# Kernel tuning notes

Hardware: AMD Instinct MI355X
Metric: run time of the kernel (lower is better)

Reference implementation:

```python
import jax, jax.numpy as jnp
import numpy as np

N = 50000        # nodes
E = 400000       # edges
F_IN = 128       # node feature dim
NEG_SLOPE = 0.2  # PyG GATConv default


def setup_inputs() -> dict:
    key = jax.random.key(0)
    ks = jax.random.split(key, 24)
    p = lambda k, shape: (jax.random.normal(k, shape, dtype=jnp.float32) * 0.1)
    return {
        "x": jax.random.normal(ks[0], (N, F_IN), dtype=jnp.float32),
        "edge_index": jax.random.randint(ks[1], (2, E), 0, N, dtype=jnp.int32),
        "edge_attr": jax.random.normal(ks[2], (E, 1), dtype=jnp.float32),
        "year": jax.random.normal(ks[3], (E, 1), dtype=jnp.float32),
        "quarter": jax.random.normal(ks[4], (E, 1), dtype=jnp.float32),
        "W1": p(ks[5], (4 * 128, F_IN)), "a1s": p(ks[6], (4, 128)), "a1d": p(ks[7], (4, 128)), "b1": jnp.zeros((512,), jnp.float32),
        "W2": p(ks[8], (4 * 32, 512)), "a2s": p(ks[9], (4, 32)), "a2d": p(ks[10], (4, 32)), "b2": jnp.zeros((128,), jnp.float32),
        "W3": p(ks[11], (1 * 8, 128)), "a3s": p(ks[12], (1, 8)), "a3d": p(ks[13], (1, 8)), "b3": jnp.zeros((8,), jnp.float32),
        # fc1: 8*2 + 1 + 2 = 19 -> 16 ; fc2: 16 -> 1
        "fc1_w": p(ks[14], (16, 19)), "fc1_b": jnp.zeros((16,), jnp.float32),
        "fc2_w": p(ks[15], (1, 16)), "fc2_b": jnp.zeros((1,), jnp.float32),
    }


def gat_conv(x, src, dst, W, a_s, a_d, b):
    """PyG GATConv (concat=True, self-loops already in src/dst, no dropout)."""
    H, C = a_s.shape
    n = x.shape[0]
    h = (x @ W.T).reshape(n, H, C)                      # [N,H,C]
    s = jnp.einsum("nhc,hc->nh", h, a_s)                # alpha_src per node
    d = jnp.einsum("nhc,hc->nh", h, a_d)                # alpha_dst per node
    e = jax.nn.leaky_relu(s[src] + d[dst], NEG_SLOPE)   # [E',H]
    m = jax.ops.segment_max(e, dst, num_segments=n)     # segment softmax over dst
    ex = jnp.exp(e - m[dst])
    den = jax.ops.segment_sum(ex, dst, num_segments=n)
    alpha = ex / den[dst]                               # [E',H]
    out = jax.ops.segment_sum(alpha[:, :, None] * h[src], dst, num_segments=n)
    return out.reshape(n, H * C) + b


def reference(x, edge_index, edge_attr, year, quarter,
              W1, a1s, a1d, b1, W2, a2s, a2d, b2, W3, a3s, a3d, b3,
              fc1_w, fc1_b, fc2_w, fc2_b):
    n = x.shape[0]
    loops = jnp.arange(n, dtype=edge_index.dtype)       # add_self_loops=True
    src = jnp.concatenate([edge_index[0], loops])
    dst = jnp.concatenate([edge_index[1], loops])
    h = jax.nn.elu(gat_conv(x, src, dst, W1, a1s, a1d, b1))
    h = jax.nn.elu(gat_conv(h, src, dst, W2, a2s, a2d, b2))
    h = jax.nn.elu(gat_conv(h, src, dst, W3, a3s, a3d, b3))
    z = jnp.concatenate([h[edge_index[0]], h[edge_index[1]], edge_attr, year, quarter], axis=1)
    z = jax.nn.relu(z @ fc1_w.T + fc1_b)
    return (z @ fc2_w.T + fc2_b).squeeze(-1)            # [E]
```

## Files before the change

kernel.cpp:

```cpp
#include <hip/hip_runtime.h>
#include <hip/hip_bf16.h>

#define NN 50000
#define EE 400000
#define EP 450000

typedef __attribute__((ext_vector_type(8))) short short8;
typedef __attribute__((ext_vector_type(4))) float f32x4;

__device__ __forceinline__ float us2f(unsigned short u) {
    unsigned int x = ((unsigned int)u) << 16;
    union { unsigned int i; float f; } c; c.i = x; return c.f;
}
__device__ __forceinline__ unsigned short f2bfu(float f) {
    union { float f; unsigned int u; } c; c.f = f;
    unsigned int r = c.u + 0x7FFFu + ((c.u >> 16) & 1u);
    return (unsigned short)(r >> 16);
}
__device__ __forceinline__ unsigned int pack2bf(float lo, float hi) {
    return (unsigned int)f2bfu(lo) | ((unsigned int)f2bfu(hi) << 16);
}
__device__ __forceinline__ float lrelu_exp(float x) {
    x = x > 0.f ? x : 0.2f * x;
    return __expf(x);
}


#define DEGB 1758
#define CVTB 512
__global__ void prep_kernel(const int* __restrict__ ei, int* __restrict__ deg,
                            const float* __restrict__ W1, const float* __restrict__ W2,
                            __hip_bfloat16* __restrict__ pw1, __hip_bfloat16* __restrict__ pw2,
                            const float* __restrict__ a1s, const float* __restrict__ a1d,
                            float* __restrict__ usd) {
    int b = blockIdx.x;
    if (b < DEGB) {
        int e = b * 256 + threadIdx.x;
        if (e >= EP) return;
        int dst = (e < EE) ? ei[EE + e] : e - EE;
        atomicAdd(&deg[dst], 1);
    } else if (b < DEGB + CVTB) {
        int i = (b - DEGB) * 256 + threadIdx.x;
        if (i < 65536) {
            int n = i >> 7, k = i & 127;
            int idx = ((n >> 4) * 4 + (k >> 5)) * 512 + ((k & 31) >> 3) * 128 + (n & 15) * 8 + (k & 7);
            pw1[idx] = __float2bfloat16(W1[i]);
        } else {
            int j = i - 65536;
            int n = j >> 9, k = j & 511;
            int idx = ((n >> 4) * 16 + (k >> 5)) * 512 + ((k & 31) >> 3) * 128 + (n & 15) * 8 + (k & 7);
            pw2[idx] = __float2bfloat16(W2[j]);
        }
    } else {
        int t = (b - DEGB - CVTB) * 256 + threadIdx.x;
        if (t >= 1024) return;
        int row = t >> 7, k = t & 127;
        int hh = row & 3;
        const float* av = (row < 4) ? (a1s + hh * 128) : (a1d + hh * 128);
        const float* wp = W1 + (size_t)(hh * 128) * 128 + k;
        float acc = 0.f;
        for (int c = 0; c < 128; c++) acc += av[c] * wp[(size_t)c * 128];
        usd[t] = acc;
    }
}

__global__ void cvtx_sd(const float* __restrict__ x, const float* __restrict__ usd,
                        __hip_bfloat16* __restrict__ xb,
                        float* __restrict__ s, float* __restrict__ d, int M) {
    __shared__ float us_s[1024];
    for (int i = threadIdx.x; i < 1024; i += 256) us_s[i] = usd[i];
    __syncthreads();
    int wave = threadIdx.x >> 6, lane = threadIdx.x & 63;
    int m0 = blockIdx.x * 64 + wave * 16;
    int r = lane & 15, quad = lane >> 4;
    int am = m0 + r; if (am >= M) am = M - 1;
    const float* xp = x + (size_t)am * 128 + quad * 8;
    float xv[32];
#pragma unroll
    for (int kk = 0; kk < 4; kk++) {
        float4 a = *(const float4*)(xp + kk * 32);
        float4 bq = *(const float4*)(xp + kk * 32 + 4);
        xv[kk*8+0]=a.x;  xv[kk*8+1]=a.y;  xv[kk*8+2]=a.z;  xv[kk*8+3]=a.w;
        xv[kk*8+4]=bq.x; xv[kk*8+5]=bq.y; xv[kk*8+6]=bq.z; xv[kk*8+7]=bq.w;
        short8 o;
        o[0]=(short)f2bfu(a.x);  o[1]=(short)f2bfu(a.y);
        o[2]=(short)f2bfu(a.z);  o[3]=(short)f2bfu(a.w);
        o[4]=(short)f2bfu(bq.x); o[5]=(short)f2bfu(bq.y);
        o[6]=(short)f2bfu(bq.z); o[7]=(short)f2bfu(bq.w);
        *(short8*)(xb + (size_t)am * 128 + quad * 8 + kk * 32) = o;
    }
    float acc[8];
#pragma unroll
    for (int o = 0; o < 8; o++) {
        const float* up = us_s + o * 128 + quad * 8;
        float a = 0.f;
#pragma unroll
        for (int kk = 0; kk < 4; kk++)
#pragma unroll
            for (int j = 0; j < 8; j++) a += xv[kk*8+j] * up[kk*32+j];
        acc[o] = a;
    }
#pragma unroll
    for (int o = 0; o < 8; o++) {
        acc[o] += __shfl_xor(acc[o], 16, 64);
        acc[o] += __shfl_xor(acc[o], 32, 64);
    }
    int m = m0 + r;
    if (quad == 0 && m < M) {
#pragma unroll
        for (int hh = 0; hh < 4; hh++) { s[m*4+hh] = acc[hh]; d[m*4+hh] = acc[4+hh]; }
    }
}

#define SCB 49
__global__ void scan1_kernel(const int* __restrict__ deg, int* __restrict__ bsum) {
    __shared__ int red[256];
    int b = blockIdx.x, t = threadIdx.x;
    int base = b * 1024 + t * 4;
    int s = 0;
    if (base + 3 < NN) { int4 v = *(const int4*)(deg + base); s = v.x + v.y + v.z + v.w; }
    else { for (int i = base; i < NN; i++) s += deg[i]; }
    red[t] = s;
    __syncthreads();
    for (int off = 128; off > 0; off >>= 1) {
        if (t < off) red[t] += red[t + off];
        __syncthreads();
    }
    if (t == 0) bsum[b] = red[0];
}

__global__ void scan2_kernel(const int* __restrict__ deg, const int* __restrict__ bsum,
                             int* __restrict__ offsets) {
    __shared__ int lsum[256];
    int b = blockIdx.x, t = threadIdx.x;
    int boff = 0;
    for (int i = 0; i < b; i++) boff += bsum[i];
    int base = b * 1024 + t * 4;
    int4 v = {0, 0, 0, 0};
    if (base + 3 < NN) v = *(const int4*)(deg + base);
    else {
        if (base < NN)     v.x = deg[base];
        if (base + 1 < NN) v.y = deg[base + 1];
        if (base + 2 < NN) v.z = deg[base + 2];
        if (base + 3 < NN) v.w = deg[base + 3];
    }
    int s = v.x + v.y + v.z + v.w;
    lsum[t] = s;
    __syncthreads();
    for (int off = 1; off < 256; off <<= 1) {
        int val = (t >= off) ? lsum[t - off] : 0;
        __syncthreads();
        lsum[t] += val;
        __syncthreads();
    }
    int ex = boff + (t ? lsum[t - 1] : 0);
    if (base < NN)     offsets[base]     = ex;
    if (base + 1 < NN) offsets[base + 1] = ex + v.x;
    if (base + 2 < NN) offsets[base + 2] = ex + v.x + v.y;
    if (base + 3 < NN) offsets[base + 3] = ex + v.x + v.y + v.z;
    if (b == SCB - 1 && t == 255) offsets[NN] = boff + lsum[255];
}

__global__ void fill_kernel(const int* __restrict__ ei, const int* __restrict__ offsets,
                            int* __restrict__ cursor,
                            const float* __restrict__ s1, const float* __restrict__ d1,
                            int* __restrict__ elist, float* __restrict__ welist) {
    int e = blockIdx.x * blockDim.x + threadIdx.x;
    if (e >= EP) return;
    int src, dst;
    if (e < EE) { src = ei[e]; dst = ei[EE + e]; } else { src = dst = e - EE; }
    int pos = atomicAdd(&cursor[dst], 1);
    int j = offsets[dst] + pos;
    elist[j] = src;
    float4 sv = *(const float4*)(s1 + (size_t)src * 4);
    float4 dv = *(const float4*)(d1 + (size_t)dst * 4);
    float4 w;
    w.x = lrelu_exp(sv.x + dv.x);
    w.y = lrelu_exp(sv.y + dv.y);
    w.z = lrelu_exp(sv.z + dv.z);
    w.w = lrelu_exp(sv.w + dv.w);
    *(float4*)(welist + (size_t)j * 4) = w;
}

__device__ __forceinline__ void acc_edge(float (&den)[4], float (&acc)[8],
                                         float4 w, unsigned int x) {
    float x0 = us2f((unsigned short)x), x1 = us2f((unsigned short)(x >> 16));
    den[0] += w.x; den[1] += w.y; den[2] += w.z; den[3] += w.w;
    acc[0] += w.x * x0; acc[1] += w.x * x1;
    acc[2] += w.y * x0; acc[3] += w.y * x1;
    acc[4] += w.z * x0; acc[5] += w.z * x1;
    acc[6] += w.w * x0; acc[7] += w.w * x1;
}

__global__ void l1_fused(
        const int* __restrict__ elist, const int* __restrict__ offsets,
        const float* __restrict__ wl,
        const __hip_bfloat16* __restrict__ xb,
        const __hip_bfloat16* __restrict__ pW1,
        const float* __restrict__ b,
        __hip_bfloat16* __restrict__ pact) {
    __shared__ unsigned short frag[16 * 520];
    int w = threadIdx.x >> 6, lane = threadIdx.x & 63;
    int m0 = blockIdx.x * 16;
    int nA = m0 + 2 * w;

    int ja  = __builtin_amdgcn_readfirstlane(offsets[nA]);
    int jA1 = __builtin_amdgcn_readfirstlane(offsets[nA + 1]);
    int jB1 = __builtin_amdgcn_readfirstlane(offsets[nA + 2]);
    int jb = jA1;

    float dA[4] = {0.f,0.f,0.f,0.f}, dB[4] = {0.f,0.f,0.f,0.f};
    float aA[8] = {0.f,0.f,0.f,0.f,0.f,0.f,0.f,0.f};
    float aB[8] = {0.f,0.f,0.f,0.f,0.f,0.f,0.f,0.f};
    const unsigned short* xp = (const unsigned short*)xb + lane * 2;
    const float4* wl4 = (const float4*)wl;

    while (ja + 2 <= jA1 && jb + 2 <= jB1) {
        int s0 = elist[ja], s1 = elist[ja + 1];
        int s2 = elist[jb], s3 = elist[jb + 1];
        float4 w0 = wl4[ja], w1 = wl4[ja + 1];
        float4 w2 = wl4[jb], w3 = wl4[jb + 1];
        unsigned int x0 = *(const unsigned int*)(xp + (size_t)s0 * 128);
        unsigned int x1 = *(const unsigned int*)(xp + (size_t)s1 * 128);
        unsigned int x2 = *(const unsigned int*)(xp + (size_t)s2 * 128);
        unsigned int x3 = *(const unsigned int*)(xp + (size_t)s3 * 128);
        acc_edge(dA, aA, w0, x0); acc_edge(dA, aA, w1, x1);
        acc_edge(dB, aB, w2, x2); acc_edge(dB, aB, w3, x3);
        ja += 2; jb += 2;
    }
    while (ja + 2 <= jA1) {
        int s0 = elist[ja], s1 = elist[ja + 1];
        float4 w0 = wl4[ja], w1 = wl4[ja + 1];
        unsigned int x0 = *(const unsigned int*)(xp + (size_t)s0 * 128);
        unsigned int x1 = *(const unsigned int*)(xp + (size_t)s1 * 128);
        acc_edge(dA, aA, w0, x0); acc_edge(dA, aA, w1, x1);
        ja += 2;
    }
    while (jb + 2 <= jB1) {
        int s0 = elist[jb], s1 = elist[jb + 1];
        float4 w0 = wl4[jb], w1 = wl4[jb + 1];
        unsigned int x0 = *(const unsigned int*)(xp + (size_t)s0 * 128);
        unsigned int x1 = *(const unsigned int*)(xp + (size_t)s1 * 128);
        acc_edge(dB, aB, w0, x0); acc_edge(dB, aB, w1, x1);
        jb += 2;
    }
    if (ja < jA1) {
        int s0 = elist[ja]; float4 w0 = wl4[ja];
        unsigned int x0 = *(const unsigned int*)(xp + (size_t)s0 * 128);
        acc_edge(dA, aA, w0, x0);
    }
    if (jb < jB1) {
        int s0 = elist[jb]; float4 w0 = wl4[jb];
        unsigned int x0 = *(const unsigned int*)(xp + (size_t)s0 * 128);
        acc_edge(dB, aB, w0, x0);
    }

    {
        int c0 = lane * 2;
        int fq = c0 >> 5;
        int sub = (c0 & 31) >> 3;
        unsigned int* f32p = (unsigned int*)frag;
        int base0 = fq * 260 + sub * 64 + (c0 & 7) / 2;
        {
            int rowp = (2 * w) ^ (sub << 2);
            int base = base0 + rowp * 4;
            float i0 = 1.f/dA[0], i1 = 1.f/dA[1], i2 = 1.f/dA[2], i3 = 1.f/dA[3];
            f32p[base]            = pack2bf(aA[0]*i0, aA[1]*i0);
            f32p[base + 4 * 260]  = pack2bf(aA[2]*i1, aA[3]*i1);
            f32p[base + 8 * 260]  = pack2bf(aA[4]*i2, aA[5]*i2);
            f32p[base + 12 * 260] = pack2bf(aA[6]*i3, aA[7]*i3);
        }
        {
            int rowp = (2 * w + 1) ^ (sub << 2);
            int base = base0 + rowp * 4;
            float i0 = 1.f/dB[0], i1 = 1.f/dB[1], i2 = 1.f/dB[2], i3 = 1.f/dB[3];
            f32p[base]            = pack2bf(aB[0]*i0, aB[1]*i0);
            f32p[base + 4 * 260]  = pack2bf(aB[2]*i1, aB[3]*i1);
            f32p[base + 8 * 260]  = pack2bf(aB[4]*i2, aB[5]*i2);
            f32p[base + 12 * 260] = pack2bf(aB[6]*i3, aB[7]*i3);
        }
    }
    __syncthreads();

    int hh = w >> 1, half = w & 1;
    int r = lane & 15, quad = lane >> 4;
    int lsub = lane >> 4, lrow = lane & 15;
    int prow = lrow ^ (lsub << 2);
    const unsigned short* fb = frag + lsub * 128 + prow * 8;
    short8 afrag[4];
#pragma unroll
    for (int kk = 0; kk < 4; kk++)
        afrag[kk] = *(const short8*)(fb + (hh * 4 + kk) * 520);
#pragma unroll
    for (int t = 0; t < 4; t++) {
        int nb = half * 64 + t * 16;
        const __hip_bfloat16* bp = pW1 + ((size_t)(hh * 8 + (nb >> 4)) * 4) * 512 + lane * 8;
        f32x4 acc = {0.f, 0.f, 0.f, 0.f};
#pragma unroll
        for (int kk = 0; kk < 4; kk++) {
            short8 bfr = *(const short8*)(bp + kk * 512);
            acc = __builtin_amdgcn_mfma_f32_16x16x32_bf16(afrag[kk], bfr, acc, 0, 0, 0);
        }
        int n0 = hh * 128 + nb;
        float bias = b[n0 + r];
        int kk2 = (n0 + r) >> 5;
        int sub2 = ((nb & 16) + r) >> 3;
        __hip_bfloat16* op = pact + ((size_t)blockIdx.x * 16 + kk2) * 512
                           + sub2 * 128 + (r & 7);
#pragma unroll
        for (int i = 0; i < 4; i++) {
            float v = acc[i] + bias;
            v = v > 0.f ? v : (__expf(v) - 1.0f);
            op[(quad * 4 + i) * 8] = __float2bfloat16(v);
        }
    }
}

__global__ void gemm_l2(const __hip_bfloat16* __restrict__ pA,
                        const __hip_bfloat16* __restrict__ pW2,
                        const float* __restrict__ as_, const float* __restrict__ ad_,
                        __hip_bfloat16* __restrict__ Cb,
                        float* __restrict__ s, float* __restrict__ d, int M) {
    int hh = threadIdx.x >> 6, lane = threadIdx.x & 63;
    int m0 = blockIdx.x * 16;
    int r = lane & 15, quad = lane >> 4;
    const __hip_bfloat16* ap  = pA + (size_t)(m0 >> 4) * 16 * 512 + lane * 8;
    const __hip_bfloat16* bp0 = pW2 + (size_t)(hh * 2) * 16 * 512 + lane * 8;
    const __hip_bfloat16* bp1 = bp0 + 16 * 512;
    f32x4 acc0 = {0.f, 0.f, 0.f, 0.f}, acc1 = {0.f, 0.f, 0.f, 0.f};
#pragma unroll
    for (int kk = 0; kk < 16; kk++) {
        short8 af = *(const short8*)(ap + kk * 512);
        short8 b0 = *(const short8*)(bp0 + kk * 512);
        short8 b1 = *(const short8*)(bp1 + kk * 512);
        acc0 = __builtin_amdgcn_mfma_f32_16x16x32_bf16(af, b0, acc0, 0, 0, 0);
        acc1 = __builtin_amdgcn_mfma_f32_16x16x32_bf16(af, b1, acc1, 0, 0, 0);
    }
    int n0 = hh * 32;
    float as0 = as_[n0 + r],      ad0 = ad_[n0 + r];
    float as1 = as_[n0 + 16 + r], ad1 = ad_[n0 + 16 + r];
    float sacc[4], dacc[4];
#pragma unroll
    for (int i = 0; i < 4; i++) {
        int m = m0 + quad * 4 + i;
        Cb[(size_t)m * 128 + n0 + r]      = __float2bfloat16(acc0[i]);
        Cb[(size_t)m * 128 + n0 + 16 + r] = __float2bfloat16(acc1[i]);
        sacc[i] = acc0[i] * as0 + acc1[i] * as1;
        dacc[i] = acc0[i] * ad0 + acc1[i] * ad1;
    }
#pragma unroll
    for (int mask = 1; mask <= 8; mask <<= 1) {
#pragma unroll
        for (int i = 0; i < 4; i++) {
            sacc[i] += __shfl_xor(sacc[i], mask, 64);
            dacc[i] += __shfl_xor(dacc[i], mask, 64);
        }
    }
    if (r == 0) {
#pragma unroll
        for (int i = 0; i < 4; i++) {
            int m = m0 + quad * 4 + i;
            s[m * 4 + hh] = sacc[i]; d[m * 4 + hh] = dacc[i];
        }
    }
}

__global__ void gather_l2_g8(const int* __restrict__ elist, const int* __restrict__ offsets,
                             const float* __restrict__ s2, const float* __restrict__ d2,
                             const __hip_bfloat16* __restrict__ h,
                             const float* __restrict__ b,
                             const float* __restrict__ W3,
                             const float* __restrict__ a3s, const float* __restrict__ a3d,
                             __hip_bfloat16* __restrict__ h3,
                             float* __restrict__ s3, float* __restrict__ d3) {
    int gid = blockIdx.x * blockDim.x + threadIdx.x;
    if (gid >= NN * 64) return;
    int node = gid >> 6;
    int lane = gid & 63;
    int c0 = lane * 2;
    int hh = lane >> 4;
    int j0 = __builtin_amdgcn_readfirstlane(offsets[node]);
    int j1 = __builtin_amdgcn_readfirstlane(offsets[node + 1]);
    float dv = d2[node * 4 + hh];
    float den = 0.f, acc0 = 0.f, acc1 = 0.f;
    const unsigned short* hp = (const unsigned short*)h + c0;
    int j = j0;
    for (; j + 4 <= j1; j += 4) {
        int sA = elist[j], sB = elist[j+1], sC = elist[j+2], sD = elist[j+3];
        float eA = s2[sA * 4 + hh] + dv, eB = s2[sB * 4 + hh] + dv;
        float eC = s2[sC * 4 + hh] + dv, eD = s2[sD * 4 + hh] + dv;
        unsigned int vA = *(const unsigned int*)(hp + (size_t)sA * 128);
        unsigned int vB = *(const unsigned int*)(hp + (size_t)sB * 128);
        unsigned int vC = *(const unsigned int*)(hp + (size_t)sC * 128);
        unsigned int vD = *(const unsigned int*)(hp + (size_t)sD * 128);
        float wA = lrelu_exp(eA), wB = lrelu_exp(eB);
        float wC = lrelu_exp(eC), wD = lrelu_exp(eD);
        den += (wA + wB) + (wC + wD);
        acc0 += wA * us2f((unsigned short)vA) + wB * us2f((unsigned short)vB)
              + wC * us2f((unsigned short)vC) + wD * us2f((unsigned short)vD);
        acc1 += wA * us2f((unsigned short)(vA >> 16)) + wB * us2f((unsigned short)(vB >> 16))
              + wC * us2f((unsigned short)(vC >> 16)) + wD * us2f((unsigned short)(vD >> 16));
    }
    for (; j < j1; j++) {
        int sE = elist[j];
        float ww = lrelu_exp(s2[sE * 4 + hh] + dv);
        unsigned int v = *(const unsigned int*)(hp + (size_t)sE * 128);
        den += ww;
        acc0 += ww * us2f((unsigned short)v);
        acc1 += ww * us2f((unsigned short)(v >> 16));
    }
    float inv = 1.0f / den;
    float v0 = acc0 * inv + b[c0];
    float v1 = acc1 * inv + b[c0 + 1];
    v0 = v0 > 0.f ? v0 : (__expf(v0) - 1.0f);
    v1 = v1 > 0.f ? v1 : (__expf(v1) - 1.0f);
    float part[8];
#pragma unroll
    for (int c = 0; c < 8; c++) {
        float2 wv = *(const float2*)(W3 + c * 128 + c0);
        part[c] = v0 * wv.x + v1 * wv.y;
    }
#pragma unroll
    for (int mask = 1; mask < 64; mask <<= 1) {
#pragma unroll
        for (int c = 0; c < 8; c++) part[c] += __shfl_xor(part[c], mask, 64);
    }
    if (lane < 8) h3[(size_t)node * 8 + lane] = __float2bfloat16(part[lane]);
    if (lane == 0) {
        float sv = 0.f, dvv = 0.f;
#pragma unroll
        for (int c = 0; c < 8; c++) { sv += part[c] * a3s[c]; dvv += part[c] * a3d[c]; }
        s3[node] = sv; d3[node] = dvv;
    }
}

__global__ void gather_l3(const int* __restrict__ elist, const int* __restrict__ offsets,
                          const float* __restrict__ s3, const float* __restrict__ d3,
                          const __hip_bfloat16* __restrict__ h,
                          const float* __restrict__ b,
                          __hip_bfloat16* __restrict__ act) {
    int gid = blockIdx.x * blockDim.x + threadIdx.x;
    if (gid >= NN * 8) return;
    int node = gid >> 3, t = gid & 7;
    int j0 = offsets[node], j1 = offsets[node + 1];
    float dnode = d3[node];
    float den = 0.f, acc = 0.f;
    const unsigned short* hp = (const unsigned short*)h + t;
    int j = j0;
    for (; j + 4 <= j1; j += 4) {
        int sA = elist[j], sB = elist[j+1], sC = elist[j+2], sD = elist[j+3];
        float wA = lrelu_exp(s3[sA] + dnode), wB = lrelu_exp(s3[sB] + dnode);
        float wC = lrelu_exp(s3[sC] + dnode), wD = lrelu_exp(s3[sD] + dnode);
        float xA = us2f(hp[(size_t)sA * 8]);
        float xB = us2f(hp[(size_t)sB * 8]);
        float xC = us2f(hp[(size_t)sC * 8]);
        float xD = us2f(hp[(size_t)sD * 8]);
        den += (wA + wB) + (wC + wD);
        acc += wA * xA + wB * xB + wC * xC + wD * xD;
    }
    for (; j < j1; j++) {
        int sE = elist[j];
        float w = lrelu_exp(s3[sE] + dnode);
        den += w;
        acc += w * us2f(hp[(size_t)sE * 8]);
    }
    float v = acc / den + b[t];
    v = v > 0.f ? v : (__expf(v) - 1.0f);
    act[(size_t)node * 8 + t] = __float2bfloat16(v);
}

__global__ void mlp_kernel(const int* __restrict__ ei,
                           const __hip_bfloat16* __restrict__ act3,
                           const float* __restrict__ ea,
                           const float* __restrict__ yr,
                           const float* __restrict__ qt,
                           const float* __restrict__ fc1w,
                           const float* __restrict__ fc1b,
                           const float* __restrict__ fc2w,
                           const float* __restrict__ fc2b,
                           float* __restrict__ outp) {
    __shared__ float w1[16 * 19], b1s[16], w2[16];
    for (int i = threadIdx.x; i < 16 * 19; i += blockDim.x) w1[i] = fc1w[i];
    if (threadIdx.x < 16) {
        b1s[threadIdx.x] = fc1b[threadIdx.x];
        w2[threadIdx.x] = fc2w[threadIdx.x];
    }
    __syncthreads();
    int e = blockIdx.x * blockDim.x + threadIdx.x;
    if (e >= EE) return;
    int src = ei[e], dst = ei[EE + e];
    short8 hs = *(const short8*)(act3 + (size_t)src * 8);
    short8 hd = *(const short8*)(act3 + (size_t)dst * 8);
    float z[19];
#pragma unroll
    for (int i = 0; i < 8; i++) z[i] = us2f((unsigned short)hs[i]);
#pragma unroll
    for (int i = 0; i < 8; i++) z[8 + i] = us2f((unsigned short)hd[i]);
    z[16] = ea[e]; z[17] = yr[e]; z[18] = qt[e];
    float acc2 = fc2b[0];
#pragma unroll
    for (int j = 0; j < 16; j++) {
        float a = b1s[j];
#pragma unroll
        for (int i = 0; i < 19; i++) a += z[i] * w1[j * 19 + i];
        a = a > 0.f ? a : 0.f;
        acc2 += a * w2[j];
    }
    outp[e] = acc2;
}

extern "C" void kernel_launch(void* const* d_in, const int* in_sizes, int n_in,
                              void* d_out, int out_size, void* d_ws, size_t ws_size,
                              hipStream_t stream) {
    const float* x    = (const float*)d_in[0];
    const int*   ei   = (const int*)d_in[1];
    const float* ea   = (const float*)d_in[2];
    const float* yr   = (const float*)d_in[3];
    const float* qt   = (const float*)d_in[4];
    const float* W1   = (const float*)d_in[5];
    const float* a1s  = (const float*)d_in[6];
    const float* a1d  = (const float*)d_in[7];
    const float* b1   = (const float*)d_in[8];
    const float* W2   = (const float*)d_in[9];
    const float* a2s  = (const float*)d_in[10];
    const float* a2d  = (const float*)d_in[11];
    const float* b2   = (const float*)d_in[12];
    const float* W3   = (const float*)d_in[13];
    const float* a3s  = (const float*)d_in[14];
    const float* a3d  = (const float*)d_in[15];
    const float* b3   = (const float*)d_in[16];
    const float* fc1w = (const float*)d_in[17];
    const float* fc1b = (const float*)d_in[18];
    const float* fc2w = (const float*)d_in[19];
    const float* fc2b = (const float*)d_in[20];
    float* outp = (float*)d_out;

    char* ws = (char*)d_ws;
    __hip_bfloat16* h_buf   = (__hip_bfloat16*)(ws);
    __hip_bfloat16* act_buf = (__hip_bfloat16*)(ws + 51200000);
    float* s_buf   = (float*)(ws + 102400000);
    float* d_buf   = (float*)(ws + 103200000);
    int*   deg     = (int*)  (ws + 104000000);
    int*   cursor  = (int*)  (ws + 104200000);
    int*   offsets = (int*)  (ws + 104400000);
    int*   elist   = (int*)  (ws + 104600016);
    __hip_bfloat16* pw1 = (__hip_bfloat16*)(ws + 106400016);
    __hip_bfloat16* pw2 = (__hip_bfloat16*)(ws + 106531088);
    float* usd  = (float*)(ws + 106662160);
    int*   bsum = (int*)  (ws + 106666256);
    float* welist = (float*)(ws + 106666512);
    float* s3_buf = (float*)(ws + 113866512);
    float* d3_buf = (float*)(ws + 114071312);
    __hip_bfloat16* xb = act_buf;

    hipMemsetAsync(deg, 0, 2 * NN * sizeof(int), stream);
    prep_kernel<<<DEGB + CVTB + 4, 256, 0, stream>>>(ei, deg, W1, W2, pw1, pw2, a1s, a1d, usd);
    scan1_kernel<<<SCB, 256, 0, stream>>>(deg, bsum);
    scan2_kernel<<<SCB, 256, 0, stream>>>(deg, bsum, offsets);
    cvtx_sd<<<(NN + 63) / 64, 256, 0, stream>>>(x, usd, xb, s_buf, d_buf, NN);
    fill_kernel<<<(EP + 255) / 256, 256, 0, stream>>>(ei, offsets, cursor, s_buf, d_buf,
                                                      elist, welist);

    l1_fused<<<NN / 16, 512, 0, stream>>>(elist, offsets, welist, xb, pw1, b1, h_buf);

    gemm_l2<<<(NN + 15) / 16, 256, 0, stream>>>(
        h_buf, pw2, a2s, a2d, act_buf, s_buf, d_buf, NN);

    gather_l2_g8<<<(NN * 64 + 255) / 256, 256, 0, stream>>>(
        elist, offsets, s_buf, d_buf, act_buf, b2, W3, a3s, a3d,
        h_buf, s3_buf, d3_buf);

    gather_l3<<<(NN * 8 + 255) / 256, 256, 0, stream>>>(
        elist, offsets, s3_buf, d3_buf, h_buf, b3, act_buf);

    mlp_kernel<<<(EE + 255) / 256, 256, 0, stream>>>(ei, act_buf, ea, yr, qt,
                                                     fc1w, fc1b, fc2w, fc2b, outp);
}
```

Before: 298.8 us.

## Fuse layer-2 GEMM into layer-1 gather kernel via shared-memory activations

The layer-1 fused kernel now keeps its ELU-activated output tile in a second shared-memory buffer. Four of its waves then run the layer-2 MFMA GEMM, including the attention source/destination dot products, directly from that buffer. This removes the round trip of the 512-wide layer-1 activation through global memory and drops the separate gemm_l2 launch. The cost is double the LDS per block, which may lower occupancy, and half the waves sit idle during the second GEMM. The layer-2 output now goes to a new workspace buffer.

After: 278.5 us. 1.07x faster.

```diff
diff --git a/kernel.cpp b/kernel.cpp
--- a/kernel.cpp
+++ b/kernel.cpp
@@ -198,8 +198,12 @@
         const __hip_bfloat16* __restrict__ xb,
         const __hip_bfloat16* __restrict__ pW1,
         const float* __restrict__ b,
-        __hip_bfloat16* __restrict__ pact) {
+        const __hip_bfloat16* __restrict__ pW2,
+        const float* __restrict__ as_, const float* __restrict__ ad_,
+        __hip_bfloat16* __restrict__ h2,
+        float* __restrict__ s2, float* __restrict__ d2) {
     __shared__ unsigned short frag[16 * 520];
+    __shared__ unsigned short act1[16 * 520];
     int w = threadIdx.x >> 6, lane = threadIdx.x & 63;
     int m0 = blockIdx.x * 16;
     int nA = m0 + 2 * w;
@@ -217,13 +221,13 @@
 
     while (ja + 2 <= jA1 && jb + 2 <= jB1) {
         int s0 = elist[ja], s1 = elist[ja + 1];
-        int s2 = elist[jb], s3 = elist[jb + 1];
+        int s2i = elist[jb], s3i = elist[jb + 1];
         float4 w0 = wl4[ja], w1 = wl4[ja + 1];
         float4 w2 = wl4[jb], w3 = wl4[jb + 1];
         unsigned int x0 = *(const unsigned int*)(xp + (size_t)s0 * 128);
         unsigned int x1 = *(const unsigned int*)(xp + (size_t)s1 * 128);
-        unsigned int x2 = *(const unsigned int*)(xp + (size_t)s2 * 128);
-        unsigned int x3 = *(const unsigned int*)(xp + (size_t)s3 * 128);
+        unsigned int x2 = *(const unsigned int*)(xp + (size_t)s2i * 128);
+        unsigned int x3 = *(const unsigned int*)(xp + (size_t)s3i * 128);
         acc_edge(dA, aA, w0, x0); acc_edge(dA, aA, w1, x1);
         acc_edge(dB, aB, w2, x2); acc_edge(dB, aB, w3, x3);
         ja += 2; jb += 2;
@@ -286,81 +290,77 @@
     int r = lane & 15, quad = lane >> 4;
     int lsub = lane >> 4, lrow = lane & 15;
     int prow = lrow ^ (lsub << 2);
-    const unsigned short* fb = frag + lsub * 128 + prow * 8;
-    short8 afrag[4];
-#pragma unroll
-    for (int kk = 0; kk < 4; kk++)
-        afrag[kk] = *(const short8*)(fb + (hh * 4 + kk) * 520);
-#pragma unroll
-    for (int t = 0; t < 4; t++) {
-        int nb = half * 64 + t * 16;
-        const __hip_bfloat16* bp = pW1 + ((size_t)(hh * 8 + (nb >> 4)) * 4) * 512 + lane * 8;
-        f32x4 acc = {0.f, 0.f, 0.f, 0.f};
-#pragma unroll
-        for (int kk = 0; kk < 4; kk++) {
-            short8 bfr = *(const short8*)(bp + kk * 512);
-            acc = __builtin_amdgcn_mfma_f32_16x16x32_bf16(afrag[kk], bfr, acc, 0, 0, 0);
-        }
-        int n0 = hh * 128 + nb;
-        float bias = b[n0 + r];
-        int kk2 = (n0 + r) >> 5;
-        int sub2 = ((nb & 16) + r) >> 3;
-        __hip_bfloat16* op = pact + ((size_t)blockIdx.x * 16 + kk2) * 512
-                           + sub2 * 128 + (r & 7);
-#pragma unroll
-        for (int i = 0; i < 4; i++) {
-            float v = acc[i] + bias;
-            v = v > 0.f ? v : (__expf(v) - 1.0f);
-            op[(quad * 4 + i) * 8] = __float2bfloat16(v);
-        }
-    }
-}
-
-__global__ void gemm_l2(const __hip_bfloat16* __restrict__ pA,
-                        const __hip_bfloat16* __restrict__ pW2,
-                        const float* __restrict__ as_, const float* __restrict__ ad_,
-                        __hip_bfloat16* __restrict__ Cb,
-                        float* __restrict__ s, float* __restrict__ d, int M) {
-    int hh = threadIdx.x >> 6, lane = threadIdx.x & 63;
-    int m0 = blockIdx.x * 16;
-    int r = lane & 15, quad = lane >> 4;
-    const __hip_bfloat16* ap  = pA + (size_t)(m0 >> 4) * 16 * 512 + lane * 8;
-    const __hip_bfloat16* bp0 = pW2 + (size_t)(hh * 2) * 16 * 512 + lane * 8;
-    const __hip_bfloat16* bp1 = bp0 + 16 * 512;
-    f32x4 acc0 = {0.f, 0.f, 0.f, 0.f}, acc1 = {0.f, 0.f, 0.f, 0.f};
-#pragma unroll
-    for (int kk = 0; kk < 16; kk++) {
-        short8 af = *(const short8*)(ap + kk * 512);
-        short8 b0 = *(const short8*)(bp0 + kk * 512);
-        short8 b1 = *(const short8*)(bp1 + kk * 512);
-        acc0 = __builtin_amdgcn_mfma_f32_16x16x32_bf16(af, b0, acc0, 0, 0, 0);
-        acc1 = __builtin_amdgcn_mfma_f32_16x16x32_bf16(af, b1, acc1, 0, 0, 0);
-    }
-    int n0 = hh * 32;
-    float as0 = as_[n0 + r],      ad0 = ad_[n0 + r];
-    float as1 = as_[n0 + 16 + r], ad1 = ad_[n0 + 16 + r];
-    float sacc[4], dacc[4];
-#pragma unroll
-    for (int i = 0; i < 4; i++) {
-        int m = m0 + quad * 4 + i;
-        Cb[(size_t)m * 128 + n0 + r]      = __float2bfloat16(acc0[i]);
-        Cb[(size_t)m * 128 + n0 + 16 + r] = __float2bfloat16(acc1[i]);
-        sacc[i] = acc0[i] * as0 + acc1[i] * as1;
-        dacc[i] = acc0[i] * ad0 + acc1[i] * ad1;
-    }
-#pragma unroll
-    for (int mask = 1; mask <= 8; mask <<= 1) {
-#pragma unroll
-        for (int i = 0; i < 4; i++) {
-            sacc[i] += __shfl_xor(sacc[i], mask, 64);
-            dacc[i] += __shfl_xor(dacc[i], mask, 64);
-        }
-    }
-    if (r == 0) {
+    {
+        const unsigned short* fb = frag + lsub * 128 + prow * 8;
+        short8 afrag[4];
+#pragma unroll
+        for (int kk = 0; kk < 4; kk++)
+            afrag[kk] = *(const short8*)(fb + (hh * 4 + kk) * 520);
+#pragma unroll
+        for (int t = 0; t < 4; t++) {
+            int nb = half * 64 + t * 16;
+            const __hip_bfloat16* bp = pW1 + ((size_t)(hh * 8 + (nb >> 4)) * 4) * 512 + lane * 8;
+            f32x4 acc = {0.f, 0.f, 0.f, 0.f};
+#pragma unroll
+            for (int kk = 0; kk < 4; kk++) {
+                short8 bfr = *(const short8*)(bp + kk * 512);
+                acc = __builtin_amdgcn_mfma_f32_16x16x32_bf16(afrag[kk], bfr, acc, 0, 0, 0);
+            }
+            int n0 = hh * 128 + nb;
+            float bias = b[n0 + r];
+            int kk2 = (n0 + r) >> 5;
+            int sub2 = ((nb & 16) + r) >> 3;
+#pragma unroll
+            for (int i = 0; i < 4; i++) {
+                float v = acc[i] + bias;
+                v = v > 0.f ? v : (__expf(v) - 1.0f);
+                int rowp2 = (quad * 4 + i) ^ (sub2 << 2);
+                act1[kk2 * 520 + sub2 * 128 + rowp2 * 8 + (r & 7)] = f2bfu(v);
+            }
+        }
+    }
+    __syncthreads();
+
+    if (w < 4) {
+        int h2h = w;
+        const __hip_bfloat16* bp0 = pW2 + (size_t)(h2h * 2) * 16 * 512 + lane * 8;
+        const __hip_bfloat16* bp1 = bp0 + 16 * 512;
+        const unsigned short* ab = act1 + lsub * 128 + prow * 8;
+        f32x4 acc0 = {0.f, 0.f, 0.f, 0.f}, acc1 = {0.f, 0.f, 0.f, 0.f};
+#pragma unroll
+        for (int kk = 0; kk < 16; kk++) {
+            short8 af = *(const short8*)(ab + kk * 520);
+            short8 b0 = *(const short8*)(bp0 + kk * 512);
+            short8 b1 = *(const short8*)(bp1 + kk * 512);
+            acc0 = __builtin_amdgcn_mfma_f32_16x16x32_bf16(af, b0, acc0, 0, 0, 0);
+            acc1 = __builtin_amdgcn_mfma_f32_16x16x32_bf16(af, b1, acc1, 0, 0, 0);
+        }
+        int n0 = h2h * 32;
+        float as0 = as_[n0 + r],      ad0 = ad_[n0 + r];
+        float as1 = as_[n0 + 16 + r], ad1 = ad_[n0 + 16 + r];
+        float sacc[4], dacc[4];
 #pragma unroll
         for (int i = 0; i < 4; i++) {
             int m = m0 + quad * 4 + i;
-            s[m * 4 + hh] = sacc[i]; d[m * 4 + hh] = dacc[i];
+            h2[(size_t)m * 128 + n0 + r]      = __float2bfloat16(acc0[i]);
+            h2[(size_t)m * 128 + n0 + 16 + r] = __float2bfloat16(acc1[i]);
+            sacc[i] = acc0[i] * as0 + acc1[i] * as1;
+            dacc[i] = acc0[i] * ad0 + acc1[i] * ad1;
+        }
+#pragma unroll
+        for (int mask = 1; mask <= 8; mask <<= 1) {
+#pragma unroll
+            for (int i = 0; i < 4; i++) {
+                sacc[i] += __shfl_xor(sacc[i], mask, 64);
+                dacc[i] += __shfl_xor(dacc[i], mask, 64);
+            }
+        }
+        if (r == 0) {
+#pragma unroll
+            for (int i = 0; i < 4; i++) {
+                int m = m0 + quad * 4 + i;
+                s2[m * 4 + h2h] = sacc[i]; d2[m * 4 + h2h] = dacc[i];
+            }
         }
     }
 }
@@ -551,6 +551,7 @@
     float* welist = (float*)(ws + 106666512);
     float* s3_buf = (float*)(ws + 113866512);
     float* d3_buf = (float*)(ws + 114071312);
+    __hip_bfloat16* h2_buf = (__hip_bfloat16*)(ws + 114276112);
     __hip_bfloat16* xb = act_buf;
 
     hipMemsetAsync(deg, 0, 2 * NN * sizeof(int), stream);
@@ -561,13 +562,11 @@
     fill_kernel<<<(EP + 255) / 256, 256, 0, stream>>>(ei, offsets, cursor, s_buf, d_buf,
                                                       elist, welist);
 
-    l1_fused<<<NN / 16, 512, 0, stream>>>(elist, offsets, welist, xb, pw1, b1, h_buf);
-
-    gemm_l2<<<(NN + 15) / 16, 256, 0, stream>>>(
-        h_buf, pw2, a2s, a2d, act_buf, s_buf, d_buf, NN);
+    l1_fused<<<NN / 16, 512, 0, stream>>>(elist, offsets, welist, xb, pw1, b1,
+                                          pw2, a2s, a2d, h2_buf, s_buf, d_buf);
 
     gather_l2_g8<<<(NN * 64 + 255) / 256, 256, 0, stream>>>(
-        elist, offsets, s_buf, d_buf, act_buf, b2, W3, a3s, a3d,
+        elist, offsets, s_buf, d_buf, h2_buf, b2, W3, a3s, a3d,
         h_buf, s3_buf, d3_buf);
 
     gather_l3<<<(NN * 8 + 255) / 256, 256, 0, stream>>>(
```
